# Optimization experiments

Hardware: AMD Instinct MI355X
Metric: run time of the kernel (lower is better)

The kernel has to match this reference:

```python
import jax, jax.numpy as jnp
import numpy as np

HEAD_DIM = 64
SCALE = HEAD_DIM ** (-0.5)


def setup_inputs() -> dict:
    key = jax.random.key(0)
    kq, kk, kv = jax.random.split(key, 3)
    B, H, S, D = 2, 12, 2048, HEAD_DIM
    query = jax.random.normal(kq, (B, H, S, D), dtype=jnp.float32)
    k = jax.random.normal(kk, (B, H, S, D), dtype=jnp.float32)
    v = jax.random.normal(kv, (B, H, S, D), dtype=jnp.float32)
    mask = jnp.ones((1, 1, S, S), dtype=jnp.int32)
    return {"query": query, "key": k, "value": v, "mask": mask}


def reference(query, key, value, mask):
    # scores: [B, H, S, S]
    scores = jnp.einsum("bhqd,bhkd->bhqk", query, key) * SCALE
    scores = jnp.where(mask == 0, -jnp.inf, scores)
    probs = jax.nn.softmax(scores, axis=-1)
    # dropout = 0.0 -> identity
    out = jnp.einsum("bhqk,bhkd->bhqd", probs, value)
    return out
```

## Files before the change

kernel.cpp:

```cpp
#include <hip/hip_runtime.h>

#define SDIM 2048
#define DDIM 64
#define NT   32
#define SCL2  (0.125f * 1.4426950408889634f)

typedef __attribute__((ext_vector_type(8))) short          bf16x8;
typedef __attribute__((ext_vector_type(8))) unsigned short ushort8;
typedef __attribute__((ext_vector_type(4))) float          f32x4;
typedef __attribute__((ext_vector_type(16))) float         f32x16;

__device__ __forceinline__ unsigned short f2bf(float x) {
    unsigned int u = __float_as_uint(x);
    u += 0x7FFFu + ((u >> 16) & 1u);
    return (unsigned short)(u >> 16);
}

__device__ __forceinline__ float fastexp2(float x) {
#if __has_builtin(__builtin_amdgcn_exp2f)
    return __builtin_amdgcn_exp2f(x);
#else
    float r;
    asm("v_exp_f32 %0, %1" : "=v"(r) : "v"(x));
    return r;
#endif
}

__global__ __launch_bounds__(256)
void prep_kv(const float* __restrict__ Kp, const float* __restrict__ Vp,
             unsigned short* __restrict__ wsK, unsigned short* __restrict__ wsV)
{
    __shared__ alignas(16) unsigned short vstage[64 * DDIM];
    const int tid = threadIdx.x;
    const int t   = blockIdx.x;
    const int bh  = blockIdx.y;
    const size_t tb   = ((size_t)bh * NT + t) * (64 * DDIM);
    const size_t gsrc = (size_t)bh * SDIM * DDIM + (size_t)t * 64 * DDIM;

    const int key = tid >> 2;
    const int d0  = (tid & 3) << 4;
    const int sw  = (key & 7) << 3;

    {
        const float* src = Kp + gsrc + key * DDIM + d0;
        float4 a0 = ((const float4*)src)[0];
        float4 a1 = ((const float4*)src)[1];
        float4 a2 = ((const float4*)src)[2];
        float4 a3 = ((const float4*)src)[3];
        ushort8 w0, w1;
        w0[0]=f2bf(a0.x); w0[1]=f2bf(a0.y); w0[2]=f2bf(a0.z); w0[3]=f2bf(a0.w);
        w0[4]=f2bf(a1.x); w0[5]=f2bf(a1.y); w0[6]=f2bf(a1.z); w0[7]=f2bf(a1.w);
        w1[0]=f2bf(a2.x); w1[1]=f2bf(a2.y); w1[2]=f2bf(a2.z); w1[3]=f2bf(a2.w);
        w1[4]=f2bf(a3.x); w1[5]=f2bf(a3.y); w1[6]=f2bf(a3.z); w1[7]=f2bf(a3.w);
        *(ushort8*)&wsK[tb + key * 64 + ( d0      ^ sw)] = w0;
        *(ushort8*)&wsK[tb + key * 64 + ((d0 + 8) ^ sw)] = w1;
    }
    {
        const float* src = Vp + gsrc + key * DDIM + d0;
        float4 a0 = ((const float4*)src)[0];
        float4 a1 = ((const float4*)src)[1];
        float4 a2 = ((const float4*)src)[2];
        float4 a3 = ((const float4*)src)[3];
        ushort8 w0, w1;
        w0[0]=f2bf(a0.x); w0[1]=f2bf(a0.y); w0[2]=f2bf(a0.z); w0[3]=f2bf(a0.w);
        w0[4]=f2bf(a1.x); w0[5]=f2bf(a1.y); w0[6]=f2bf(a1.z); w0[7]=f2bf(a1.w);
        w1[0]=f2bf(a2.x); w1[1]=f2bf(a2.y); w1[2]=f2bf(a2.z); w1[3]=f2bf(a2.w);
        w1[4]=f2bf(a3.x); w1[5]=f2bf(a3.y); w1[6]=f2bf(a3.z); w1[7]=f2bf(a3.w);
        *(ushort8*)&vstage[key * 64 + ( d0      ^ sw)] = w0;
        *(ushort8*)&vstage[key * 64 + ((d0 + 8) ^ sw)] = w1;
    }
    __syncthreads();
    {
        const int d   = tid >> 2;
        const int k0  = (tid & 3) << 4;
        const int st  = k0 >> 5;
        const int kh  = (k0 >> 4) & 1;
        const int dsw = (d >> 1) & 3;
        unsigned short vals[16];
        #pragma unroll
        for (int m = 0; m < 16; ++m) {
            const int k = k0 + m;
            vals[m] = vstage[k * 64 + (d ^ ((k & 7) << 3))];
        }
        const size_t vbase = tb + st * 2048 + d * 32;
        #pragma unroll
        for (int hh = 0; hh < 2; ++hh) {
            ushort8 o;
            #pragma unroll
            for (int j = 0; j < 8; ++j)
                o[j] = vals[(j & 3) + 4 * hh + 8 * (j >> 2)];
            *(ushort8*)&wsV[vbase + (((2 * kh + hh) ^ dsw) << 3)] = o;
        }
    }
}

__global__ __launch_bounds__(256, 4)
void attn64_main(const float* __restrict__ Qp,
                 const unsigned short* __restrict__ wsK,
                 const unsigned short* __restrict__ wsV,
                 float* __restrict__ Op, int bhpx)
{
    __shared__ float combO[3 * 64 * 32];
    __shared__ float combL[3 * 64];

    const int tid  = threadIdx.x;
    const int lane = tid & 63;
    const int par  = tid >> 6;
    const int l5   = lane & 31;
    const int h    = lane >> 5;

    const int blk = blockIdx.x;
    int bh, qt;
    if (bhpx) {
        const int loc = blk >> 3;
        bh = (blk & 7) * bhpx + (loc >> 6);
        qt = loc & 63;
    } else {
        bh = blk >> 6;
        qt = blk & 63;
    }

    const unsigned short* Kt = wsK + (size_t)bh * (SDIM * DDIM);
    const unsigned short* Vt = wsV + (size_t)bh * (SDIM * DDIM);

    bf16x8 qf[4];
    {
        const float* Qb = Qp + (size_t)bh * SDIM * DDIM;
        const int qrow = qt * 32 + l5;
        #pragma unroll
        for (int ks = 0; ks < 4; ++ks) {
            const float* src = Qb + (size_t)qrow * DDIM + ks * 16 + h * 8;
            float4 a = ((const float4*)src)[0];
            float4 b = ((const float4*)src)[1];
            bf16x8 tq;
            tq[0] = (short)f2bf(a.x * SCL2); tq[1] = (short)f2bf(a.y * SCL2);
            tq[2] = (short)f2bf(a.z * SCL2); tq[3] = (short)f2bf(a.w * SCL2);
            tq[4] = (short)f2bf(b.x * SCL2); tq[5] = (short)f2bf(b.y * SCL2);
            tq[6] = (short)f2bf(b.z * SCL2); tq[7] = (short)f2bf(b.w * SCL2);
            qf[ks] = tq;
        }
    }

    int kaddr[4];
    #pragma unroll
    for (int ks = 0; ks < 4; ++ks)
        kaddr[ks] = l5 * 64 + ((ks * 16 + h * 8) ^ ((l5 & 7) << 3));
    int vaddr[2][2];
    #pragma unroll
    for (int kh = 0; kh < 2; ++kh)
        #pragma unroll
        for (int dh = 0; dh < 2; ++dh) {
            const int d = dh * 32 + l5;
            vaddr[kh][dh] = d * 32 + (((2 * kh + h) ^ ((d >> 1) & 3)) << 3);
        }

    f32x16 oacc0, oacc1;
    #pragma unroll
    for (int i = 0; i < 16; ++i) { oacc0[i] = 0.f; oacc1[i] = 0.f; }
    float rs = 0.f;

    const unsigned short* kp = Kt + par * 2048;
    const unsigned short* vp = Vt + par * 2048;

    bf16x8 kf[4];
    #pragma unroll
    for (int ks = 0; ks < 4; ++ks) kf[ks] = *(const bf16x8*)&kp[kaddr[ks]];

    #pragma unroll 1
    for (int it = 0; it < 16; ++it) {
        bf16x8 v00 = *(const bf16x8*)&vp[vaddr[0][0]];
        bf16x8 v01 = *(const bf16x8*)&vp[vaddr[0][1]];
        bf16x8 v10 = *(const bf16x8*)&vp[vaddr[1][0]];
        bf16x8 v11 = *(const bf16x8*)&vp[vaddr[1][1]];

        f32x16 s;
        #pragma unroll
        for (int i = 0; i < 16; ++i) s[i] = 0.f;
        __builtin_amdgcn_s_setprio(1);
        #pragma unroll
        for (int ks = 0; ks < 4; ++ks)
            s = __builtin_amdgcn_mfma_f32_32x32x16_bf16(kf[ks], qf[ks], s, 0, 0, 0);
        __builtin_amdgcn_s_setprio(0);

        kp += 8192;
        if (it < 15) {
            #pragma unroll
            for (int ks = 0; ks < 4; ++ks) kf[ks] = *(const bf16x8*)&kp[kaddr[ks]];
        }

        union { unsigned int u[8]; bf16x8 v[2]; } P;
        #pragma unroll
        for (int i = 0; i < 8; ++i) {
            const float p0 = fastexp2(s[2 * i]);
            const float p1 = fastexp2(s[2 * i + 1]);
            unsigned int r;
            asm("v_cvt_pk_bf16_f32 %0, %1, %2" : "=v"(r) : "v"(p0), "v"(p1));
            P.u[i] = r;
            rs += __uint_as_float(r << 16) + __uint_as_float(r & 0xFFFF0000u);
        }

        __builtin_amdgcn_s_setprio(1);
        oacc0 = __builtin_amdgcn_mfma_f32_32x32x16_bf16(v00, P.v[0], oacc0, 0, 0, 0);
        oacc1 = __builtin_amdgcn_mfma_f32_32x32x16_bf16(v01, P.v[0], oacc1, 0, 0, 0);
        oacc0 = __builtin_amdgcn_mfma_f32_32x32x16_bf16(v10, P.v[1], oacc0, 0, 0, 0);
        oacc1 = __builtin_amdgcn_mfma_f32_32x32x16_bf16(v11, P.v[1], oacc1, 0, 0, 0);
        __builtin_amdgcn_s_setprio(0);

        vp += 8192;
    }

    rs += __shfl_xor(rs, 32);

    __syncthreads();
    const int sx = lane & 7;
    if (par) {
        float* d = &combO[((par - 1) * 64 + lane) * 32];
        #pragma unroll
        for (int c = 0; c < 8; ++c) {
            f32x4 q;
            if (c < 4) q = f32x4{ oacc0[4*c], oacc0[4*c+1], oacc0[4*c+2], oacc0[4*c+3] };
            else       q = f32x4{ oacc1[4*(c-4)], oacc1[4*(c-4)+1], oacc1[4*(c-4)+2], oacc1[4*(c-4)+3] };
            *(f32x4*)&d[(c ^ sx) << 2] = q;
        }
        combL[(par - 1) * 64 + lane] = rs;
    }
    __syncthreads();
    if (par == 0) {
        #pragma unroll
        for (int sl = 0; sl < 3; ++sl) {
            const float* d = &combO[(sl * 64 + lane) * 32];
            #pragma unroll
            for (int c = 0; c < 8; ++c) {
                f32x4 q = *(const f32x4*)&d[(c ^ sx) << 2];
                if (c < 4) {
                    oacc0[4*c] += q[0]; oacc0[4*c+1] += q[1];
                    oacc0[4*c+2] += q[2]; oacc0[4*c+3] += q[3];
                } else {
                    oacc1[4*(c-4)] += q[0]; oacc1[4*(c-4)+1] += q[1];
                    oacc1[4*(c-4)+2] += q[2]; oacc1[4*(c-4)+3] += q[3];
                }
            }
            rs += combL[sl * 64 + lane];
        }
        const float inv = 1.f / rs;
        const int q = qt * 32 + l5;
        float* dst = Op + (size_t)bh * SDIM * DDIM + (size_t)q * DDIM;
        #pragma unroll
        for (int rg = 0; rg < 4; ++rg) {
            float4 o0 = { oacc0[4*rg] * inv, oacc0[4*rg+1] * inv,
                          oacc0[4*rg+2] * inv, oacc0[4*rg+3] * inv };
            *(float4*)&dst[8 * rg + 4 * h] = o0;
            float4 o1 = { oacc1[4*rg] * inv, oacc1[4*rg+1] * inv,
                          oacc1[4*rg+2] * inv, oacc1[4*rg+3] * inv };
            *(float4*)&dst[32 + 8 * rg + 4 * h] = o1;
        }
    }
}

typedef __attribute__((ext_vector_type(4))) short bf16x4;

__global__ __launch_bounds__(256)
void attn64_fallback(const float* __restrict__ Qp, const float* __restrict__ Kp,
                     const float* __restrict__ Vp, float* __restrict__ Op)
{
    __shared__ alignas(16) unsigned short kls[64 * DDIM];
    __shared__ alignas(16) unsigned short vls[DDIM * 64];
    __shared__ alignas(16) unsigned short pls[4][16 * 64];

    const int tid  = threadIdx.x;
    const int lane = tid & 63;
    const int wave = tid >> 6;
    const int lo4  = lane & 15;
    const int hi2  = lane >> 4;
    const int qt = blockIdx.x;
    const int bh = blockIdx.y;

    const size_t base = (size_t)bh * SDIM * DDIM;
    const float* Qb = Qp + base;
    const float* Kb = Kp + base;
    const float* Vb = Vp + base;
    float*       Ob = Op + base;

    bf16x8 qf[2];
    {
        const int qrow = qt * 64 + wave * 16 + lo4;
        #pragma unroll
        for (int ks = 0; ks < 2; ++ks) {
            const float* src = Qb + (size_t)qrow * DDIM + ks * 32 + hi2 * 8;
            float4 a = ((const float4*)src)[0];
            float4 b = ((const float4*)src)[1];
            bf16x8 tq;
            tq[0] = (short)f2bf(a.x * SCL2); tq[1] = (short)f2bf(a.y * SCL2);
            tq[2] = (short)f2bf(a.z * SCL2); tq[3] = (short)f2bf(a.w * SCL2);
            tq[4] = (short)f2bf(b.x * SCL2); tq[5] = (short)f2bf(b.y * SCL2);
            tq[6] = (short)f2bf(b.z * SCL2); tq[7] = (short)f2bf(b.w * SCL2);
            qf[ks] = tq;
        }
    }

    float mrow[4], lrow[4];
    f32x4 oacc[4];
    #pragma unroll
    for (int r = 0; r < 4; ++r) { mrow[r] = -1e30f; lrow[r] = 0.f; }
    #pragma unroll
    for (int n = 0; n < 4; ++n) oacc[n] = f32x4{0.f, 0.f, 0.f, 0.f};

    for (int t0 = 0; t0 < SDIM; t0 += 64) {
        __syncthreads();
        {
            const int key = tid >> 2;
            const int d0  = (tid & 3) << 4;
            const float* src = Kb + (size_t)(t0 + key) * DDIM + d0;
            float4 a0 = ((const float4*)src)[0];
            float4 a1 = ((const float4*)src)[1];
            float4 a2 = ((const float4*)src)[2];
            float4 a3 = ((const float4*)src)[3];
            ushort8 w0, w1;
            w0[0]=f2bf(a0.x); w0[1]=f2bf(a0.y); w0[2]=f2bf(a0.z); w0[3]=f2bf(a0.w);
            w0[4]=f2bf(a1.x); w0[5]=f2bf(a1.y); w0[6]=f2bf(a1.z); w0[7]=f2bf(a1.w);
            w1[0]=f2bf(a2.x); w1[1]=f2bf(a2.y); w1[2]=f2bf(a2.z); w1[3]=f2bf(a2.w);
            w1[4]=f2bf(a3.x); w1[5]=f2bf(a3.y); w1[6]=f2bf(a3.z); w1[7]=f2bf(a3.w);
            const int sw = (key & 7) << 3;
            *(ushort8*)&kls[key * 64 + ( d0      ^ sw)] = w0;
            *(ushort8*)&kls[key * 64 + ((d0 + 8) ^ sw)] = w1;
        }
        {
            const int key = lane;
            const int d0  = wave << 4;
            const float* src = Vb + (size_t)(t0 + key) * DDIM + d0;
            float4 b0 = ((const float4*)src)[0];
            float4 b1 = ((const float4*)src)[1];
            float4 b2 = ((const float4*)src)[2];
            float4 b3 = ((const float4*)src)[3];
            float vv[16] = { b0.x,b0.y,b0.z,b0.w, b1.x,b1.y,b1.z,b1.w,
                             b2.x,b2.y,b2.z,b2.w, b3.x,b3.y,b3.z,b3.w };
            #pragma unroll
            for (int j = 0; j < 16; ++j) {
                const int d = d0 + j;
                vls[d * 64 + (key ^ ((d & 7) << 3))] = f2bf(vv[j]);
            }
        }
        __syncthreads();

        f32x4 s[4];
        #pragma unroll
        for (int n = 0; n < 4; ++n) s[n] = f32x4{0.f, 0.f, 0.f, 0.f};
        #pragma unroll
        for (int ks = 0; ks < 2; ++ks) {
            const int kb = ks * 32 + hi2 * 8;
            #pragma unroll
            for (int n = 0; n < 4; ++n) {
                const int key = lo4 + 16 * n;
                bf16x8 b = *(const bf16x8*)&kls[key * 64 + (kb ^ ((key & 7) << 3))];
                s[n] = __builtin_amdgcn_mfma_f32_16x16x32_bf16(qf[ks], b, s[n], 0, 0, 0);
            }
        }
        #pragma unroll
        for (int r = 0; r < 4; ++r) {
            float tmax = fmaxf(fmaxf(s[0][r], s[1][r]), fmaxf(s[2][r], s[3][r]));
            tmax = fmaxf(tmax, __shfl_xor(tmax, 1));
            tmax = fmaxf(tmax, __shfl_xor(tmax, 2));
            tmax = fmaxf(tmax, __shfl_xor(tmax, 4));
            tmax = fmaxf(tmax, __shfl_xor(tmax, 8));
            const float mn   = fmaxf(mrow[r], tmax);
            const float corr = exp2f(mrow[r] - mn);
            mrow[r] = mn;
            float rs = 0.f;
            #pragma unroll
            for (int n = 0; n < 4; ++n) {
                const float p = exp2f(s[n][r] - mn);
                s[n][r] = p;
                rs += p;
            }
            rs += __shfl_xor(rs, 1);
            rs += __shfl_xor(rs, 2);
            rs += __shfl_xor(rs, 4);
            rs += __shfl_xor(rs, 8);
            lrow[r] = lrow[r] * corr + rs;
            #pragma unroll
            for (int n = 0; n < 4; ++n) oacc[n][r] *= corr;
        }
        #pragma unroll
        for (int r = 0; r < 4; ++r) {
            const int q  = hi2 * 4 + r;
            const int sw = (q & 7) << 3;
            #pragma unroll
            for (int n = 0; n < 4; ++n)
                pls[wave][q * 64 + ((lo4 + 16 * n) ^ sw)] = f2bf(s[n][r]);
        }
        __syncthreads();
        #pragma unroll
        for (int ks = 0; ks < 2; ++ks) {
            const int kb = ks * 32 + hi2 * 8;
            bf16x8 a = *(const bf16x8*)&pls[wave][lo4 * 64 + (kb ^ ((lo4 & 7) << 3))];
            #pragma unroll
            for (int n = 0; n < 4; ++n) {
                const int d = 16 * n + lo4;
                bf16x8 b = *(const bf16x8*)&vls[d * 64 + (kb ^ ((d & 7) << 3))];
                oacc[n] = __builtin_amdgcn_mfma_f32_16x16x32_bf16(a, b, oacc[n], 0, 0, 0);
            }
        }
    }
    #pragma unroll
    for (int r = 0; r < 4; ++r) {
        const float inv = 1.f / lrow[r];
        const int q = qt * 64 + wave * 16 + hi2 * 4 + r;
        float* dst = Ob + (size_t)q * DDIM;
        #pragma unroll
        for (int n = 0; n < 4; ++n)
            dst[16 * n + lo4] = oacc[n][r] * inv;
    }
}

extern "C" void kernel_launch(void* const* d_in, const int* in_sizes, int n_in,
                              void* d_out, int out_size, void* d_ws, size_t ws_size,
                              hipStream_t stream) {
    const float* Q = (const float*)d_in[0];
    const float* K = (const float*)d_in[1];
    const float* V = (const float*)d_in[2];
    float* O = (float*)d_out;
    const int BH = in_sizes[0] / (SDIM * DDIM);
    const size_t need = 2ull * BH * SDIM * DDIM * sizeof(unsigned short);

    if (ws_size >= need) {
        unsigned short* wsK = (unsigned short*)d_ws;
        unsigned short* wsV = wsK + (size_t)BH * SDIM * DDIM;
        const int bhpx = (BH % 8 == 0) ? (BH / 8) : 0;
        prep_kv<<<dim3(NT, BH), dim3(256), 0, stream>>>(K, V, wsK, wsV);
        attn64_main<<<dim3(BH * 64), dim3(256), 0, stream>>>(Q, wsK, wsV, O, bhpx);
    } else {
        attn64_fallback<<<dim3(SDIM / 64, BH), dim3(256), 0, stream>>>(Q, K, V, O);
    }
}
```

Baseline: 56.87 us.

## Pre-pack K/V tiles in fragment order for fully coalesced lane-contiguous loads

The prep kernel now writes K and V bf16 tiles in MFMA fragment order, so each lane's 8-element fragment sits at lane*8 within a 512-element block. The main attention loop can then load K and V fragments with simple contiguous per-lane offsets instead of XOR-swizzled address arrays. This removes per-lane address registers and makes each wavefront's global loads a single contiguous 1 KB span. Correctness depends on the prep layout matching exactly what the MFMA operand mapping expects.

```diff
diff --git a/kernel.cpp b/kernel.cpp
--- a/kernel.cpp
+++ b/kernel.cpp
@@ -39,7 +39,6 @@
 
     const int key = tid >> 2;
     const int d0  = (tid & 3) << 4;
-    const int sw  = (key & 7) << 3;
 
     {
         const float* src = Kp + gsrc + key * DDIM + d0;
@@ -52,8 +51,12 @@
         w0[4]=f2bf(a1.x); w0[5]=f2bf(a1.y); w0[6]=f2bf(a1.z); w0[7]=f2bf(a1.w);
         w1[0]=f2bf(a2.x); w1[1]=f2bf(a2.y); w1[2]=f2bf(a2.z); w1[3]=f2bf(a2.w);
         w1[4]=f2bf(a3.x); w1[5]=f2bf(a3.y); w1[6]=f2bf(a3.z); w1[7]=f2bf(a3.w);
-        *(ushort8*)&wsK[tb + key * 64 + ( d0      ^ sw)] = w0;
-        *(ushort8*)&wsK[tb + key * 64 + ((d0 + 8) ^ sw)] = w1;
+        const int st = key >> 5;
+        const int l5 = key & 31;
+        const int ks = d0 >> 4;
+        unsigned short* base = wsK + tb + st * 2048 + ks * 512;
+        *(ushort8*)&base[l5 * 8]        = w0;
+        *(ushort8*)&base[(32 + l5) * 8] = w1;
     }
     {
         const float* src = Vp + gsrc + key * DDIM + d0;
@@ -66,6 +69,7 @@
         w0[4]=f2bf(a1.x); w0[5]=f2bf(a1.y); w0[6]=f2bf(a1.z); w0[7]=f2bf(a1.w);
         w1[0]=f2bf(a2.x); w1[1]=f2bf(a2.y); w1[2]=f2bf(a2.z); w1[3]=f2bf(a2.w);
         w1[4]=f2bf(a3.x); w1[5]=f2bf(a3.y); w1[6]=f2bf(a3.z); w1[7]=f2bf(a3.w);
+        const int sw = (key & 7) << 3;
         *(ushort8*)&vstage[key * 64 + ( d0      ^ sw)] = w0;
         *(ushort8*)&vstage[key * 64 + ((d0 + 8) ^ sw)] = w1;
     }
@@ -75,21 +79,22 @@
         const int k0  = (tid & 3) << 4;
         const int st  = k0 >> 5;
         const int kh  = (k0 >> 4) & 1;
-        const int dsw = (d >> 1) & 3;
+        const int dh  = d >> 5;
+        const int l5v = d & 31;
         unsigned short vals[16];
         #pragma unroll
         for (int m = 0; m < 16; ++m) {
             const int k = k0 + m;
             vals[m] = vstage[k * 64 + (d ^ ((k & 7) << 3))];
         }
-        const size_t vbase = tb + st * 2048 + d * 32;
-        #pragma unroll
-        for (int hh = 0; hh < 2; ++hh) {
+        unsigned short* base = wsV + tb + st * 2048 + (kh * 2 + dh) * 512;
+        #pragma unroll
+        for (int h = 0; h < 2; ++h) {
             ushort8 o;
             #pragma unroll
             for (int j = 0; j < 8; ++j)
-                o[j] = vals[(j & 3) + 4 * hh + 8 * (j >> 2)];
-            *(ushort8*)&wsV[vbase + (((2 * kh + hh) ^ dsw) << 3)] = o;
+                o[j] = vals[(j & 3) + 4 * h + 8 * (j >> 2)];
+            *(ushort8*)&base[(h * 32 + l5v) * 8] = o;
         }
     }
 }
@@ -141,37 +146,24 @@
         }
     }
 
-    int kaddr[4];
-    #pragma unroll
-    for (int ks = 0; ks < 4; ++ks)
-        kaddr[ks] = l5 * 64 + ((ks * 16 + h * 8) ^ ((l5 & 7) << 3));
-    int vaddr[2][2];
-    #pragma unroll
-    for (int kh = 0; kh < 2; ++kh)
-        #pragma unroll
-        for (int dh = 0; dh < 2; ++dh) {
-            const int d = dh * 32 + l5;
-            vaddr[kh][dh] = d * 32 + (((2 * kh + h) ^ ((d >> 1) & 3)) << 3);
-        }
-
     f32x16 oacc0, oacc1;
     #pragma unroll
     for (int i = 0; i < 16; ++i) { oacc0[i] = 0.f; oacc1[i] = 0.f; }
     float rs = 0.f;
 
-    const unsigned short* kp = Kt + par * 2048;
-    const unsigned short* vp = Vt + par * 2048;
+    const unsigned short* kp = Kt + par * 2048 + lane * 8;
+    const unsigned short* vp = Vt + par * 2048 + lane * 8;
 
     bf16x8 kf[4];
     #pragma unroll
-    for (int ks = 0; ks < 4; ++ks) kf[ks] = *(const bf16x8*)&kp[kaddr[ks]];
+    for (int ks = 0; ks < 4; ++ks) kf[ks] = *(const bf16x8*)&kp[ks * 512];
 
     #pragma unroll 1
     for (int it = 0; it < 16; ++it) {
-        bf16x8 v00 = *(const bf16x8*)&vp[vaddr[0][0]];
-        bf16x8 v01 = *(const bf16x8*)&vp[vaddr[0][1]];
-        bf16x8 v10 = *(const bf16x8*)&vp[vaddr[1][0]];
-        bf16x8 v11 = *(const bf16x8*)&vp[vaddr[1][1]];
+        bf16x8 v00 = *(const bf16x8*)&vp[0 * 512];
+        bf16x8 v01 = *(const bf16x8*)&vp[1 * 512];
+        bf16x8 v10 = *(const bf16x8*)&vp[2 * 512];
+        bf16x8 v11 = *(const bf16x8*)&vp[3 * 512];
 
         f32x16 s;
         #pragma unroll
@@ -185,7 +177,7 @@
         kp += 8192;
         if (it < 15) {
             #pragma unroll
-            for (int ks = 0; ks < 4; ++ks) kf[ks] = *(const bf16x8*)&kp[kaddr[ks]];
+            for (int ks = 0; ks < 4; ++ks) kf[ks] = *(const bf16x8*)&kp[ks * 512];
         }
 
         union { unsigned int u[8]; bf16x8 v[2]; } P;
```

After: 50.88 us. 10.5% less time.
